# Performance work log

Measured on AMD Instinct MI355X. Metric: run time of the kernel, lower is better.

The kernel has to match this reference:

```python
import jax, jax.numpy as jnp
import numpy as np
from jax import lax


def run_gru(seq, w_ih, w_hh, b_ih, b_hh):
    """PyTorch-convention GRU. seq: (T, N, E) -> outputs (T, N, H), h0 = 0."""
    H = w_hh.shape[1]
    gx = jnp.einsum('tne,ge->tng', seq, w_ih) + b_ih  # (T, N, 3H), precomputed input gates

    def step(h, gx_t):
        gh = h @ w_hh.T + b_hh
        xr, xz, xn = jnp.split(gx_t, 3, axis=-1)
        hr, hz, hn = jnp.split(gh, 3, axis=-1)
        r = jax.nn.sigmoid(xr + hr)
        z = jax.nn.sigmoid(xz + hz)
        n = jnp.tanh(xn + r * hn)
        h_new = (1.0 - z) * n + z * h
        return h_new, h_new

    h0 = jnp.zeros((seq.shape[1], H), dtype=seq.dtype)
    _, hs = lax.scan(step, h0, gx)
    return hs


def setup_inputs() -> dict:
    key = jax.random.key(0)
    ks = jax.random.split(key, 20)
    B, T, I, E, Ha, Hb, O = 32, 64, 256, 256, 256, 256, 1
    s = 0.05
    return {
        'x': jax.random.normal(ks[0], (B, T, I), dtype=jnp.float32),
        'emb_w': jax.random.normal(ks[1], (E, I), dtype=jnp.float32) * s,
        'emb_b': jax.random.normal(ks[2], (E,), dtype=jnp.float32) * s,
        'a_wih': jax.random.normal(ks[3], (3 * Ha, E), dtype=jnp.float32) * s,
        'a_whh': jax.random.normal(ks[4], (3 * Ha, Ha), dtype=jnp.float32) * s,
        'a_bih': jax.random.normal(ks[5], (3 * Ha,), dtype=jnp.float32) * s,
        'a_bhh': jax.random.normal(ks[6], (3 * Ha,), dtype=jnp.float32) * s,
        'b_wih': jax.random.normal(ks[7], (3 * Hb, E), dtype=jnp.float32) * s,
        'b_whh': jax.random.normal(ks[8], (3 * Hb, Hb), dtype=jnp.float32) * s,
        'b_bih': jax.random.normal(ks[9], (3 * Hb,), dtype=jnp.float32) * s,
        'b_bhh': jax.random.normal(ks[10], (3 * Hb,), dtype=jnp.float32) * s,
        'alpha_w': jax.random.normal(ks[11], (1, Ha), dtype=jnp.float32) * s,
        'alpha_b': jax.random.normal(ks[12], (1,), dtype=jnp.float32) * s,
        'beta_w': jax.random.normal(ks[13], (E, Hb), dtype=jnp.float32) * s,
        'beta_b': jax.random.normal(ks[14], (E,), dtype=jnp.float32) * s,
        'out_w': jax.random.normal(ks[15], (O, E), dtype=jnp.float32) * s,
        'out_b': jax.random.normal(ks[16], (O,), dtype=jnp.float32) * s,
    }


def reference(x, emb_w, emb_b, a_wih, a_whh, a_bih, a_bhh,
              b_wih, b_whh, b_bih, b_bhh, alpha_w, alpha_b,
              beta_w, beta_b, out_w, out_b):
    B, T, I = x.shape
    P = T - 1  # prefix lengths 1..T-1
    xt = jnp.transpose(x, (1, 0, 2))               # (T, B, I) time-major
    emb = jnp.einsum('tbi,ei->tbe', xt, emb_w) + emb_b  # (T, B, E)
    E = emb.shape[-1]

    # Reversed prefix p (length t=p+1): rev[p, k] = emb[p - k] for k < t, else 0.
    idx = jnp.arange(P)[:, None] - jnp.arange(T)[None, :]   # (P, T)
    valid = idx >= 0
    idxc = jnp.clip(idx, 0)
    rev = jnp.where(valid[:, :, None, None], emb[idxc], 0.0)  # (P, T, B, E)

    seq = jnp.transpose(rev, (1, 0, 2, 3)).reshape(T, P * B, E)  # (T, P*B, E)
    ha = run_gru(seq, a_wih, a_whh, a_bih, a_bhh)  # (T, P*B, Ha)
    hb = run_gru(seq, b_wih, b_whh, b_bih, b_bhh)  # (T, P*B, Hb)
    ha = jnp.transpose(ha.reshape(T, P, B, -1), (1, 0, 2, 3))  # (P, T, B, Ha)
    hb = jnp.transpose(hb.reshape(T, P, B, -1), (1, 0, 2, 3))

    # flip back within each prefix (same index map), then * 0.5 as in the source
    rows = jnp.arange(P)[:, None]
    fa = ha[rows, idxc] * 0.5   # (P, T, B, Ha); positions >= t are junk, masked below
    fb = hb[rows, idxc] * 0.5

    pre = jnp.einsum('ptbh,h->ptb', fa, alpha_w[0]) + alpha_b[0]
    logits = jnp.where(valid[:, :, None], pre, -jnp.inf)
    alpha = jax.nn.softmax(logits, axis=1)                       # softmax over time per prefix
    beta = jnp.tanh(jnp.einsum('ptbh,eh->ptbe', fb, beta_w) + beta_b)  # (P, T, B, E)

    # context: c_t = sum_j alpha * beta * emb[:t]  (alpha is 0 outside prefix)
    c = jnp.einsum('ptb,ptbe,tbe->pbe', alpha, beta, emb)        # (P, B, E)
    pred = (c @ out_w.T + out_b)                                  # (P, B, 1)
    pred = jnp.transpose(pred, (1, 0, 2))                         # (B, P, 1)

    # contribution weights; w_emb / w_out enter via .data in torch (no grad)
    w_emb = lax.stop_gradient(emb_w)
    w_out0 = lax.stop_gradient(out_w)[0]
    e = jnp.einsum('ptbe,e,ei->ptbi', beta, w_out0, w_emb)        # (P, T, B, I)
    denom = jnp.arange(1, P + 1, dtype=x.dtype)[:, None, None]    # mean over t visits
    g = jnp.einsum('ptb,ptbi,tbi->pbi', alpha, e, xt) / denom     # (P, B, I)
    weight = jnp.transpose(g, (1, 0, 2))                          # (B, P, I)
    return pred, weight
```

## Files before the change

### kernel.cpp

```cpp
#include <hip/hip_runtime.h>
#include <math.h>

#define B_   32
#define T_   64
#define P_   63
#define E_   256

typedef _Float16 half8 __attribute__((ext_vector_type(8)));
typedef _Float16 half4 __attribute__((ext_vector_type(4)));
typedef float    f32x4 __attribute__((ext_vector_type(4)));

__device__ __forceinline__ float sigmoidf_(float x) { return 1.0f / (1.0f + __expf(-x)); }
__device__ __forceinline__ float tanhfast_(float x) { float e = __expf(2.0f*x); return 1.0f - 2.0f/(e + 1.0f); }

__device__ __forceinline__ void barrier_lds_() {
    asm volatile("" ::: "memory");
    asm volatile("s_waitcnt lgkmcnt(0)" ::: "memory");
    __builtin_amdgcn_s_barrier();
    asm volatile("" ::: "memory");
}

__global__ __launch_bounds__(64) void k_prep(
    const float* __restrict__ awhh, const float* __restrict__ bwhh,
    const float* __restrict__ awih, const float* __restrict__ bwih,
    const float* __restrict__ beta_w, const float* __restrict__ emb_w, const float* __restrict__ out_w,
    _Float16* __restrict__ wfa, _Float16* __restrict__ wfb,
    _Float16* __restrict__ wifa, _Float16* __restrict__ wifb,
    _Float16* __restrict__ bwf, _Float16* __restrict__ mf)
{
    int bid = blockIdx.x, l = threadIdx.x;
    if (bid < 1664) {
        const float* W; _Float16* dst; float scale = 1.0f; int r;
        if (bid < 384)       { W = awhh;   dst = wfa;  r = bid; }
        else if (bid < 768)  { W = bwhh;   dst = wfb;  r = bid - 384; }
        else if (bid < 1152) { W = awih;   dst = wifa; r = bid - 768; }
        else if (bid < 1536) { W = bwih;   dst = wifb; r = bid - 1152; }
        else                 { W = beta_w; dst = bwf;  r = bid - 1536; scale = 0.5f; }
        int ot = r >> 3, kc = r & 7;
        int orow = ot * 16 + (l & 15);
        int c0   = kc * 32 + (l >> 4) * 8;
        half8 v;
        #pragma unroll
        for (int j = 0; j < 8; ++j) v[j] = (_Float16)(scale * W[(size_t)orow * 256 + c0 + j]);
        *reinterpret_cast<half8*>(&dst[((size_t)r * 64 + l) * 8]) = v;
    } else {
        int r = bid - 1664;
        int ot = r >> 3, kc = r & 7;
        int i  = ot * 16 + (l & 15);
        int e0 = kc * 32 + (l >> 4) * 8;
        half8 v;
        #pragma unroll
        for (int j = 0; j < 8; ++j) v[j] = (_Float16)(out_w[e0 + j] * emb_w[(size_t)(e0 + j) * 256 + i]);
        *reinterpret_cast<half8*>(&mf[((size_t)r * 64 + l) * 8]) = v;
    }
}

__global__ __launch_bounds__(256) void k_emb(const float* __restrict__ x,
                                             const float* __restrict__ emb_w,
                                             const float* __restrict__ emb_b,
                                             const float* __restrict__ out_w,
                                             _Float16* __restrict__ embh,
                                             _Float16* __restrict__ ewh,
                                             _Float16* __restrict__ xh) {
    int r0 = blockIdx.x * 8;
    int tid = threadIdx.x;
    __shared__ float xs[8][E_];
    for (int rr = 0; rr < 8; ++rr) {
        int row = r0 + rr, t = row >> 5, b = row & 31;
        float xv = x[((size_t)b * T_ + t) * E_ + tid];
        xs[rr][tid] = xv;
        xh[((size_t)b * T_ + t) * E_ + tid] = (_Float16)xv;
    }
    __syncthreads();
    float acc[8];
    #pragma unroll
    for (int rr = 0; rr < 8; ++rr) acc[rr] = 0.f;
    const float* wr = emb_w + (size_t)tid * E_;
    for (int c = 0; c < 256; c += 4) {
        float4 wv = *reinterpret_cast<const float4*>(wr + c);
        #pragma unroll
        for (int rr = 0; rr < 8; ++rr) {
            float4 ev = *reinterpret_cast<const float4*>(&xs[rr][c]);
            acc[rr] += wv.x * ev.x + wv.y * ev.y + wv.z * ev.z + wv.w * ev.w;
        }
    }
    float eb = emb_b[tid], ow = out_w[tid];
    #pragma unroll
    for (int rr = 0; rr < 8; ++rr) {
        float v = acc[rr] + eb;
        embh[(size_t)(r0 + rr) * E_ + tid] = (_Float16)v;
        ewh[(size_t)(r0 + rr) * E_ + tid]  = (_Float16)(v * ow);
    }
}

__global__ __launch_bounds__(512, 2) void k_gates2(
    const _Float16* __restrict__ embh,
    const _Float16* __restrict__ wifa, const _Float16* __restrict__ wifb,
    const float* __restrict__ abih, const float* __restrict__ abhh,
    const float* __restrict__ bbih, const float* __restrict__ bbhh,
    _Float16* __restrict__ gpa, _Float16* __restrict__ gpb)
{
    __shared__ _Float16 esw[32 * E_];
    int bid = blockIdx.x;
    int g = bid >> 6, t = bid & 63;
    const _Float16* wif = g ? wifb : wifa;
    const float* bih = g ? bbih : abih;
    const float* bhh = g ? bbhh : abhh;
    _Float16* gp = g ? gpb : gpa;
    int tid = threadIdx.x, w = tid >> 6, l = tid & 63, lg = l >> 4, lr = l & 15;

    #pragma unroll
    for (int q = 0; q < 2; ++q) {
        int idx = q * 512 + tid;
        int b = idx >> 5, e0 = (idx & 31) * 8;
        half8 v = *reinterpret_cast<const half8*>(&embh[((size_t)t * 32 + b) * E_ + e0]);
        *reinterpret_cast<half8*>(&esw[b * E_ + (e0 ^ ((b & 7) << 3))]) = v;
    }
    half8 aw[3][2][8];
    #pragma unroll
    for (int g3 = 0; g3 < 3; ++g3)
        #pragma unroll
        for (int i = 0; i < 2; ++i)
            #pragma unroll
            for (int kc = 0; kc < 8; ++kc)
                aw[g3][i][kc] = *reinterpret_cast<const half8*>(
                    &wif[(((size_t)(g3 * 16 + 2 * w + i) * 8 + kc) * 64 + l) * 8]);
    f32x4 acc[3][2][2];
    #pragma unroll
    for (int g3 = 0; g3 < 3; ++g3)
        #pragma unroll
        for (int i = 0; i < 2; ++i)
            #pragma unroll
            for (int rt = 0; rt < 2; ++rt)
                #pragma unroll
                for (int j = 0; j < 4; ++j) {
                    int d = g3 * 256 + 32 * w + 16 * i + lg * 4 + j;
                    acc[g3][i][rt][j] = bih[d] + ((g3 < 2) ? bhh[d] : 0.f);
                }
    __syncthreads();
    #pragma unroll
    for (int kc = 0; kc < 8; ++kc) {
        half8 eb[2];
        #pragma unroll
        for (int rt = 0; rt < 2; ++rt)
            eb[rt] = *reinterpret_cast<const half8*>(
                &esw[(rt * 16 + lr) * E_ + ((kc * 32 + lg * 8) ^ ((lr & 7) << 3))]);
        #pragma unroll
        for (int g3 = 0; g3 < 3; ++g3)
            #pragma unroll
            for (int i = 0; i < 2; ++i)
                #pragma unroll
                for (int rt = 0; rt < 2; ++rt)
                    acc[g3][i][rt] = __builtin_amdgcn_mfma_f32_16x16x32_f16(
                        aw[g3][i][kc], eb[rt], acc[g3][i][rt], 0, 0, 0);
    }
    #pragma unroll
    for (int g3 = 0; g3 < 3; ++g3)
        #pragma unroll
        for (int rt = 0; rt < 2; ++rt) {
            half8 v;
            #pragma unroll
            for (int i = 0; i < 2; ++i)
                #pragma unroll
                for (int j = 0; j < 4; ++j) v[i * 4 + j] = (_Float16)acc[g3][i][rt][j];
            *reinterpret_cast<half8*>(
                &gp[((((size_t)t * 2 + rt) * 8 + w) * 3 + g3) * 512 + l * 8]) = v;
        }
}

__global__ __launch_bounds__(512, 2) void k_gru_f(
    const _Float16* __restrict__ gpa, const _Float16* __restrict__ gpb,
    const _Float16* __restrict__ wfa, const _Float16* __restrict__ wfb,
    const float* __restrict__ abhh, const float* __restrict__ bbhh,
    const float* __restrict__ alpha_w, const float* __restrict__ alpha_b,
    float* __restrict__ pre, _Float16* __restrict__ hstore)
{
    extern __shared__ char smem[];
    half8*    wlds = reinterpret_cast<half8*>(smem);
    _Float16* hsp  = reinterpret_cast<_Float16*>(smem + 98304);
    float*    red  = reinterpret_cast<float*>(smem + 98304 + 16384);

    int bid = blockIdx.x;
    int p   = 62 - (bid >> 2);
    int g   = (bid >> 1) & 1;
    int bh  = bid & 1;
    int tid = threadIdx.x;
    int w = tid >> 6, l = tid & 63, lg = l >> 4, lr = l & 15;
    const _Float16* gp  = g ? gpb : gpa;
    const _Float16* wf  = g ? wfb : wfa;
    const float*    bhh = g ? bbhh : abhh;

    half8 wreg[3][2][6];
    #pragma unroll
    for (int g3 = 0; g3 < 3; ++g3)
        #pragma unroll
        for (int i = 0; i < 2; ++i) {
            int ot = g3 * 16 + 2 * w + i;
            #pragma unroll
            for (int kc = 0; kc < 6; ++kc)
                wreg[g3][i][kc] = *reinterpret_cast<const half8*>(&wf[((size_t)(ot * 8 + kc) * 64 + l) * 8]);
        }
    #pragma unroll
    for (int q = 0; q < 12; ++q) {
        int idx = q * 512 + tid;
        int ot = idx >> 7, kcs = (idx >> 6) & 1, l2 = idx & 63;
        wlds[idx] = *reinterpret_cast<const half8*>(&wf[((size_t)(ot * 8 + 6 + kcs) * 64 + l2) * 8]);
    }
    float bhn[2][4], awv[2][4];
    #pragma unroll
    for (int i = 0; i < 2; ++i)
        #pragma unroll
        for (int j = 0; j < 4; ++j) {
            int d = 32 * w + 16 * i + lg * 4 + j;
            bhn[i][j] = bhh[512 + d];
            awv[i][j] = alpha_w[d];
        }
    float ab = alpha_b[0];
    float hreg[2][4];
    #pragma unroll
    for (int i = 0; i < 2; ++i)
        #pragma unroll
        for (int j = 0; j < 4; ++j) hreg[i][j] = 0.f;
    __syncthreads();

    size_t tri = (size_t)p * (p + 1) / 2;

    for (int k = 0; k <= p; ++k) {
        int t_in = p - k;
        int wr = k & 1, rb = wr ^ 1;
        if (k > 0 && g == 0 && tid < 16) {
            float s = 0.f;
            #pragma unroll
            for (int q = 0; q < 8; ++q) s += red[(rb * 16 + tid) * 8 + q];
            pre[((size_t)p * T_ + (t_in + 1)) * B_ + bh * 16 + tid] = 0.5f * s + ab;
        }
        half8 gch[3];
        {
            const _Float16* gq = gp + (((size_t)(t_in * 2 + bh) * 8 + w) * 3) * 512 + l * 8;
            #pragma unroll
            for (int c = 0; c < 3; ++c)
                gch[c] = *reinterpret_cast<const half8*>(gq + (size_t)c * 512);
        }
        f32x4 acc[3][2];
        #pragma unroll
        for (int g3 = 0; g3 < 3; ++g3)
            #pragma unroll
            for (int i = 0; i < 2; ++i)
                #pragma unroll
                for (int j = 0; j < 4; ++j) acc[g3][i][j] = 0.f;
        if (k > 0) {
            half8 bhv[2];
            {
                int cb = (lg * 8) ^ ((lr & 7) << 3);
                bhv[0] = *reinterpret_cast<const half8*>(&hsp[(rb * 16 + lr) * 256 + cb]);
            }
            #pragma unroll
            for (int kc = 0; kc < 8; ++kc) {
                if (kc < 7) {
                    int cb = ((kc + 1) * 32 + lg * 8) ^ ((lr & 7) << 3);
                    bhv[(kc + 1) & 1] = *reinterpret_cast<const half8*>(&hsp[(rb * 16 + lr) * 256 + cb]);
                }
                if (kc < 6) {
                    #pragma unroll
                    for (int g3 = 0; g3 < 3; ++g3)
                        #pragma unroll
                        for (int i = 0; i < 2; ++i)
                            acc[g3][i] = __builtin_amdgcn_mfma_f32_16x16x32_f16(
                                wreg[g3][i][kc], bhv[kc & 1], acc[g3][i], 0, 0, 0);
                } else {
                    #pragma unroll
                    for (int g3 = 0; g3 < 3; ++g3)
                        #pragma unroll
                        for (int i = 0; i < 2; ++i) {
                            half8 wlv = wlds[((g3 * 16 + 2 * w + i) * 2 + (kc - 6)) * 64 + l];
                            acc[g3][i] = __builtin_amdgcn_mfma_f32_16x16x32_f16(
                                wlv, bhv[kc & 1], acc[g3][i], 0, 0, 0);
                        }
                }
            }
        }
        _Float16* hdst = hstore + ((tri + (size_t)k) * B_ + bh * 16 + lr) * (size_t)E_ + 32 * w + lg * 4;
        #pragma unroll
        for (int i = 0; i < 2; ++i) {
            half4 hh;
            #pragma unroll
            for (int j = 0; j < 4; ++j) {
                int e = i * 4 + j;
                float rg = sigmoidf_(acc[0][i][j] + (float)gch[0][e]);
                float zg = sigmoidf_(acc[1][i][j] + (float)gch[1][e]);
                float ng = tanhfast_((float)gch[2][e] + rg * (acc[2][i][j] + bhn[i][j]));
                float h  = (1.f - zg) * ng + zg * hreg[i][j];
                hreg[i][j] = h;
                hh[j] = (_Float16)h;
            }
            int ce = (32 * w + 16 * i + lg * 4) ^ ((lr & 7) << 3);
            *reinterpret_cast<half4*>(&hsp[(wr * 16 + lr) * 256 + ce]) = hh;
            if (g) *reinterpret_cast<half4*>(hdst + 16 * i) = hh;
        }
        if (!g) {
            float pa = 0.f;
            #pragma unroll
            for (int i = 0; i < 2; ++i)
                #pragma unroll
                for (int j = 0; j < 4; ++j) pa += hreg[i][j] * awv[i][j];
            pa += __shfl_xor(pa, 16, 64);
            pa += __shfl_xor(pa, 32, 64);
            if (l < 16) red[(wr * 16 + l) * 8 + w] = pa;
        }
        barrier_lds_();
    }
    if (g == 0 && tid < 16) {
        int wl = p & 1;
        float s = 0.f;
        #pragma unroll
        for (int q = 0; q < 8; ++q) s += red[(wl * 16 + tid) * 8 + q];
        pre[((size_t)p * T_ + 0) * B_ + bh * 16 + tid] = 0.5f * s + ab;
    }
}

__global__ __launch_bounds__(512, 2) void k_att3(
    const _Float16* __restrict__ hH,
    const _Float16* __restrict__ bwf, const _Float16* __restrict__ mf,
    const float* __restrict__ beta_b,
    const float* __restrict__ pre,
    const _Float16* __restrict__ ewh, const _Float16* __restrict__ xh,
    const float* __restrict__ out_b,
    float* __restrict__ out)
{
    extern __shared__ char smem[];
    _Float16* hs   = reinterpret_cast<_Float16*>(smem);
    _Float16* es2  = reinterpret_cast<_Float16*>(smem + 32768);
    _Float16* xs2  = reinterpret_cast<_Float16*>(smem + 65536);
    float*    alds = reinterpret_cast<float*>(smem + 98304);
    float*    red2 = reinterpret_cast<float*>(smem + 98304 + 256);
    int tid = threadIdx.x, w = tid >> 6, l = tid & 63, lg = l >> 4, lr = l & 15;

    half8 aw2[2][8], am2[2][8];
    #pragma unroll
    for (int i = 0; i < 2; ++i)
        #pragma unroll
        for (int kc = 0; kc < 8; ++kc) {
            size_t fo = (((size_t)(2 * w + i) * 8 + kc) * 64 + l) * 8;
            aw2[i][kc] = *reinterpret_cast<const half8*>(&bwf[fo]);
            am2[i][kc] = *reinterpret_cast<const half8*>(&mf[fo]);
        }
    float bb2[2][4];
    #pragma unroll
    for (int i = 0; i < 2; ++i)
        #pragma unroll
        for (int j = 0; j < 4; ++j)
            bb2[i][j] = beta_b[(2 * w + i) * 16 + lg * 4 + j];
    float ob = out_b[0];

    for (int it = 0; it < 8; ++it) {
        int pair = blockIdx.x * 8 + it;
        int p = pair >> 5, b = pair & 31;
        size_t tri = (size_t)p * (p + 1) / 2;
        #pragma unroll
        for (int q = 0; q < 4; ++q) {
            int idx = q * 512 + tid;
            int k = idx >> 5, e0 = (idx & 31) * 8;
            int sw = e0 ^ ((k & 7) << 3);
            half8 hv, ev;
            if (k <= p) {
                hv = *reinterpret_cast<const half8*>(&hH[((tri + (size_t)(p - k)) * B_ + b) * 256 + e0]);
                ev = *reinterpret_cast<const half8*>(&ewh[((size_t)k * B_ + b) * 256 + e0]);
            } else {
                #pragma unroll
                for (int j = 0; j < 8; ++j) { hv[j] = (_Float16)0.f; ev[j] = (_Float16)0.f; }
            }
            *reinterpret_cast<half8*>(&hs[k * 256 + sw])  = hv;
            *reinterpret_cast<half8*>(&es2[k * 256 + sw]) = ev;
            *reinterpret_cast<half8*>(&xs2[k * 256 + sw]) =
                *reinterpret_cast<const half8*>(&xh[((size_t)b * T_ + k) * 256 + e0]);
        }
        if (tid < 64) {
            float v = (tid <= p) ? pre[((size_t)p * T_ + tid) * B_ + b] : -3.4e38f;
            float m = v;
            #pragma unroll
            for (int off = 32; off > 0; off >>= 1) m = fmaxf(m, __shfl_xor(m, off, 64));
            float e = (tid <= p) ? __expf(v - m) : 0.f;
            float s = e;
            #pragma unroll
            for (int off = 32; off > 0; off >>= 1) s += __shfl_xor(s, off, 64);
            alds[tid] = e / s;
        }
        __syncthreads();
        f32x4 acc2[2][4];
        #pragma unroll
        for (int i = 0; i < 2; ++i)
            #pragma unroll
            for (int rt = 0; rt < 4; ++rt)
                #pragma unroll
                for (int j = 0; j < 4; ++j) acc2[i][rt][j] = bb2[i][j];
        #pragma unroll
        for (int kc = 0; kc < 8; ++kc) {
            half8 hb[4];
            #pragma unroll
            for (int rt = 0; rt < 4; ++rt)
                hb[rt] = *reinterpret_cast<const half8*>(&hs[(rt * 16 + lr) * 256 + ((kc * 32 + lg * 8) ^ ((lr & 7) << 3))]);
            #pragma unroll
            for (int i = 0; i < 2; ++i)
                #pragma unroll
                for (int rt = 0; rt < 4; ++rt)
                    acc2[i][rt] = __builtin_amdgcn_mfma_f32_16x16x32_f16(aw2[i][kc], hb[rt], acc2[i][rt], 0, 0, 0);
        }
        float pv = 0.f;
        half4 ureg[2][4];
        #pragma unroll
        for (int i = 0; i < 2; ++i)
            #pragma unroll
            for (int rt = 0; rt < 4; ++rt) {
                int k = rt * 16 + lr;
                float al = alds[k];
                int d0 = (2 * w + i) * 16 + lg * 4;
                half4 ev4 = *reinterpret_cast<const half4*>(&es2[k * 256 + (d0 ^ ((lr & 7) << 3))]);
                #pragma unroll
                for (int j = 0; j < 4; ++j) {
                    float u = al * tanhfast_(acc2[i][rt][j]);
                    ureg[i][rt][j] = (_Float16)u;
                    pv += u * (float)ev4[j];
                }
            }
        __syncthreads();
        #pragma unroll
        for (int i = 0; i < 2; ++i)
            #pragma unroll
            for (int rt = 0; rt < 4; ++rt) {
                int k = rt * 16 + lr;
                int d0 = (2 * w + i) * 16 + lg * 4;
                *reinterpret_cast<half4*>(&hs[k * 256 + (d0 ^ ((lr & 7) << 3))]) = ureg[i][rt];
            }
        #pragma unroll
        for (int off = 1; off < 64; off <<= 1) pv += __shfl_xor(pv, off, 64);
        if (l == 0) red2[w] = pv;
        __syncthreads();
        if (tid == 0) {
            float s = 0.f;
            #pragma unroll
            for (int q = 0; q < 8; ++q) s += red2[q];
            out[(size_t)b * P_ + p] = s + ob;
        }
        f32x4 a2[2][4];
        #pragma unroll
        for (int i = 0; i < 2; ++i)
            #pragma unroll
            for (int rt = 0; rt < 4; ++rt)
                #pragma unroll
                for (int j = 0; j < 4; ++j) a2[i][rt][j] = 0.f;
        #pragma unroll
        for (int kc = 0; kc < 8; ++kc) {
            half8 ub[4];
            #pragma unroll
            for (int rt = 0; rt < 4; ++rt)
                ub[rt] = *reinterpret_cast<const half8*>(&hs[(rt * 16 + lr) * 256 + ((kc * 32 + lg * 8) ^ ((lr & 7) << 3))]);
            #pragma unroll
            for (int i = 0; i < 2; ++i)
                #pragma unroll
                for (int rt = 0; rt < 4; ++rt)
                    a2[i][rt] = __builtin_amdgcn_mfma_f32_16x16x32_f16(am2[i][kc], ub[rt], a2[i][rt], 0, 0, 0);
        }
        float r4[2][4];
        #pragma unroll
        for (int i = 0; i < 2; ++i)
            #pragma unroll
            for (int j = 0; j < 4; ++j) r4[i][j] = 0.f;
        #pragma unroll
        for (int i = 0; i < 2; ++i)
            #pragma unroll
            for (int rt = 0; rt < 4; ++rt) {
                int k = rt * 16 + lr;
                int i0 = (2 * w + i) * 16 + lg * 4;
                half4 xv4 = *reinterpret_cast<const half4*>(&xs2[k * 256 + (i0 ^ ((lr & 7) << 3))]);
                #pragma unroll
                for (int j = 0; j < 4; ++j) r4[i][j] += a2[i][rt][j] * (float)xv4[j];
            }
        #pragma unroll
        for (int off = 1; off < 16; off <<= 1)
            #pragma unroll
            for (int i = 0; i < 2; ++i)
                #pragma unroll
                for (int j = 0; j < 4; ++j) r4[i][j] += __shfl_xor(r4[i][j], off, 64);
        if (lr == 0) {
            float inv = 1.f / (float)(p + 1);
            #pragma unroll
            for (int i = 0; i < 2; ++i) {
                f32x4 v;
                #pragma unroll
                for (int j = 0; j < 4; ++j) v[j] = r4[i][j] * inv;
                *reinterpret_cast<f32x4*>(&out[2016 + ((size_t)b * P_ + p) * 256 + (2 * w + i) * 16 + lg * 4]) = v;
            }
        }
        __syncthreads();
    }
}

extern "C" void kernel_launch(void* const* d_in, const int* in_sizes, int n_in,
                              void* d_out, int out_size, void* d_ws, size_t ws_size,
                              hipStream_t stream) {
    const float* x       = (const float*)d_in[0];
    const float* emb_w   = (const float*)d_in[1];
    const float* emb_b   = (const float*)d_in[2];
    const float* a_wih   = (const float*)d_in[3];
    const float* a_whh   = (const float*)d_in[4];
    const float* a_bih   = (const float*)d_in[5];
    const float* a_bhh   = (const float*)d_in[6];
    const float* b_wih   = (const float*)d_in[7];
    const float* b_whh   = (const float*)d_in[8];
    const float* b_bih   = (const float*)d_in[9];
    const float* b_bhh   = (const float*)d_in[10];
    const float* alpha_w = (const float*)d_in[11];
    const float* alpha_b = (const float*)d_in[12];
    const float* beta_w  = (const float*)d_in[13];
    const float* beta_b  = (const float*)d_in[14];
    const float* out_w   = (const float*)d_in[15];
    const float* out_b   = (const float*)d_in[16];
    float* out = (float*)d_out;

    float* ws = (float*)d_ws;
    _Float16* embh = (_Float16*)ws;
    _Float16* ewh  = embh + 524288;
    _Float16* xh   = ewh  + 524288;
    _Float16* gpa  = xh   + 524288;
    _Float16* gpb  = gpa  + 1572864;
    float* pre     = (float*)(gpb + 1572864);
    _Float16* wfa  = (_Float16*)(pre + 129024);
    _Float16* wfb  = wfa + 196608;
    _Float16* wifa = wfb + 196608;
    _Float16* wifb = wifa + 196608;
    _Float16* bwf  = wifb + 196608;
    _Float16* mf   = bwf + 65536;
    _Float16* hH   = mf  + 65536;

    const int GRU_LDS = 98304 + 16384 + 1024;
    (void)hipFuncSetAttribute((const void*)k_gru_f,
                              hipFuncAttributeMaxDynamicSharedMemorySize, GRU_LDS);
    const int ATT_LDS = 98304 + 256 + 32;
    (void)hipFuncSetAttribute((const void*)k_att3,
                              hipFuncAttributeMaxDynamicSharedMemorySize, ATT_LDS);

    k_prep<<<1792, 64, 0, stream>>>(a_whh, b_whh, a_wih, b_wih, beta_w, emb_w, out_w,
                                    wfa, wfb, wifa, wifb, bwf, mf);
    k_emb<<<256, 256, 0, stream>>>(x, emb_w, emb_b, out_w, embh, ewh, xh);
    k_gates2<<<128, 512, 0, stream>>>(embh, wifa, wifb, a_bih, a_bhh, b_bih, b_bhh, gpa, gpb);
    k_gru_f<<<252, 512, GRU_LDS, stream>>>(gpa, gpb, wfa, wfb, a_bhh, b_bhh,
                                           alpha_w, alpha_b, pre, hH);
    k_att3<<<252, 512, ATT_LDS, stream>>>(hH, bwf, mf, beta_b, pre, ewh, xh, out_b, out);
}
```

Baseline: 287.0 us.

## Prefetch next pair's global tiles into registers during attention compute

Inside the attention kernel, the global loads of hidden states, ewh, x and pre-logits for the next (prefix, batch) pair are issued into registers right after the first barrier. They then overlap with the current pair's MFMA and reduction work. The __syncthreads calls are replaced with a custom barrier that waits only on LDS counters, so in-flight global loads are not drained at each barrier. This adds about 12 half8 registers per thread, which may pressure occupancy under the 512x2 launch bound.

Result: slower. 333.5 us (+16.2%).

```diff
diff --git a/kernel.cpp b/kernel.cpp
--- a/kernel.cpp
+++ b/kernel.cpp
@@ -318,7 +318,7 @@
     }
 }
 
-__global__ __launch_bounds__(512, 2) void k_att3(
+__global__ __launch_bounds__(512, 2) void k_att4(
     const _Float16* __restrict__ hH,
     const _Float16* __restrict__ bwf, const _Float16* __restrict__ mf,
     const float* __restrict__ beta_b,
@@ -352,30 +352,48 @@
             bb2[i][j] = beta_b[(2 * w + i) * 16 + lg * 4 + j];
     float ob = out_b[0];
 
+    half8 sh[4], se[4], sx[4];
+    float spre;
+
+#define ISSUE(PAIR) do {                                                              \
+    int p_ = (PAIR) >> 5, b_ = (PAIR) & 31;                                           \
+    size_t tri_ = (size_t)p_ * (p_ + 1) / 2;                                          \
+    _Pragma("unroll")                                                                 \
+    for (int q_ = 0; q_ < 4; ++q_) {                                                  \
+        int idx_ = q_ * 512 + tid;                                                    \
+        int k_ = idx_ >> 5, e0_ = (idx_ & 31) * 8;                                    \
+        if (k_ <= p_) {                                                               \
+            sh[q_] = *reinterpret_cast<const half8*>(                                 \
+                &hH[((tri_ + (size_t)(p_ - k_)) * B_ + b_) * 256 + e0_]);             \
+            se[q_] = *reinterpret_cast<const half8*>(                                 \
+                &ewh[((size_t)k_ * B_ + b_) * 256 + e0_]);                            \
+        } else {                                                                      \
+            _Pragma("unroll")                                                         \
+            for (int j_ = 0; j_ < 8; ++j_) { sh[q_][j_] = (_Float16)0.f;              \
+                                             se[q_][j_] = (_Float16)0.f; }            \
+        }                                                                             \
+        sx[q_] = *reinterpret_cast<const half8*>(                                     \
+            &xh[((size_t)b_ * T_ + k_) * 256 + e0_]);                                 \
+    }                                                                                 \
+    spre = (tid < 64 && tid <= p_) ? pre[((size_t)p_ * T_ + tid) * B_ + b_] : -3.4e38f; \
+} while (0)
+
+    ISSUE(blockIdx.x * 8);
+
     for (int it = 0; it < 8; ++it) {
         int pair = blockIdx.x * 8 + it;
         int p = pair >> 5, b = pair & 31;
-        size_t tri = (size_t)p * (p + 1) / 2;
         #pragma unroll
         for (int q = 0; q < 4; ++q) {
             int idx = q * 512 + tid;
             int k = idx >> 5, e0 = (idx & 31) * 8;
             int sw = e0 ^ ((k & 7) << 3);
-            half8 hv, ev;
-            if (k <= p) {
-                hv = *reinterpret_cast<const half8*>(&hH[((tri + (size_t)(p - k)) * B_ + b) * 256 + e0]);
-                ev = *reinterpret_cast<const half8*>(&ewh[((size_t)k * B_ + b) * 256 + e0]);
-            } else {
-                #pragma unroll
-                for (int j = 0; j < 8; ++j) { hv[j] = (_Float16)0.f; ev[j] = (_Float16)0.f; }
-            }
-            *reinterpret_cast<half8*>(&hs[k * 256 + sw])  = hv;
-            *reinterpret_cast<half8*>(&es2[k * 256 + sw]) = ev;
-            *reinterpret_cast<half8*>(&xs2[k * 256 + sw]) =
-                *reinterpret_cast<const half8*>(&xh[((size_t)b * T_ + k) * 256 + e0]);
+            *reinterpret_cast<half8*>(&hs[k * 256 + sw])  = sh[q];
+            *reinterpret_cast<half8*>(&es2[k * 256 + sw]) = se[q];
+            *reinterpret_cast<half8*>(&xs2[k * 256 + sw]) = sx[q];
         }
         if (tid < 64) {
-            float v = (tid <= p) ? pre[((size_t)p * T_ + tid) * B_ + b] : -3.4e38f;
+            float v = spre;
             float m = v;
             #pragma unroll
             for (int off = 32; off > 0; off >>= 1) m = fmaxf(m, __shfl_xor(m, off, 64));
@@ -385,7 +403,8 @@
             for (int off = 32; off > 0; off >>= 1) s += __shfl_xor(s, off, 64);
             alds[tid] = e / s;
         }
-        __syncthreads();
+        barrier_lds_();
+        if (it < 7) ISSUE(pair + 1);
         f32x4 acc2[2][4];
         #pragma unroll
         for (int i = 0; i < 2; ++i)
@@ -422,7 +441,7 @@
                     pv += u * (float)ev4[j];
                 }
             }
-        __syncthreads();
+        barrier_lds_();
         #pragma unroll
         for (int i = 0; i < 2; ++i)
             #pragma unroll
@@ -434,7 +453,7 @@
         #pragma unroll
         for (int off = 1; off < 64; off <<= 1) pv += __shfl_xor(pv, off, 64);
         if (l == 0) red2[w] = pv;
-        __syncthreads();
+        barrier_lds_();
         if (tid == 0) {
             float s = 0.f;
             #pragma unroll
@@ -491,8 +510,9 @@
                 *reinterpret_cast<f32x4*>(&out[2016 + ((size_t)b * P_ + p) * 256 + (2 * w + i) * 16 + lg * 4]) = v;
             }
         }
-        __syncthreads();
-    }
+        barrier_lds_();
+    }
+#undef ISSUE
 }
 
 extern "C" void kernel_launch(void* const* d_in, const int* in_sizes, int n_in,
@@ -536,7 +556,7 @@
     (void)hipFuncSetAttribute((const void*)k_gru_f,
                               hipFuncAttributeMaxDynamicSharedMemorySize, GRU_LDS);
     const int ATT_LDS = 98304 + 256 + 32;
-    (void)hipFuncSetAttribute((const void*)k_att3,
+    (void)hipFuncSetAttribute((const void*)k_att4,
                               hipFuncAttributeMaxDynamicSharedMemorySize, ATT_LDS);
 
     k_prep<<<1792, 64, 0, stream>>>(a_whh, b_whh, a_wih, b_wih, beta_w, emb_w, out_w,
@@ -545,5 +565,5 @@
     k_gates2<<<128, 512, 0, stream>>>(embh, wifa, wifb, a_bih, a_bhh, b_bih, b_bhh, gpa, gpb);
     k_gru_f<<<252, 512, GRU_LDS, stream>>>(gpa, gpb, wfa, wfb, a_bhh, b_bhh,
                                            alpha_w, alpha_b, pre, hH);
-    k_att3<<<252, 512, ATT_LDS, stream>>>(hH, bwf, mf, beta_b, pre, ewh, xh, out_b, out);
-}
+    k_att4<<<252, 512, ATT_LDS, stream>>>(hH, bwf, mf, beta_b, pre, ewh, xh, out_b, out);
+}
```

## Process full batch per GRU block instead of splitting batch halves

Applied to the files above, without the earlier changes.

Each k_gru_f block now handles all 32 batch rows (two 16-row tiles) rather than one half, halving the grid from 252 to 126 blocks. The recurrent weights held in registers and LDS are reused across both row tiles, which doubles MFMA work per weight load and halves redundant weight staging. The gate-precompute layout in k_gates2 is permuted so that both row tiles sit next to each other, and LDS for hidden state and the reduction buffer is doubled. The trade-off is fewer blocks to fill the CUs and a longer serial time per block, plus higher register pressure from the doubled accumulators.

Result: slower. 582.5 us (+102.9%).

```diff
diff --git a/kernel.cpp b/kernel.cpp
--- a/kernel.cpp
+++ b/kernel.cpp
@@ -164,7 +164,7 @@
                 #pragma unroll
                 for (int j = 0; j < 4; ++j) v[i * 4 + j] = (_Float16)acc[g3][i][rt][j];
             *reinterpret_cast<half8*>(
-                &gp[((((size_t)t * 2 + rt) * 8 + w) * 3 + g3) * 512 + l * 8]) = v;
+                &gp[((((size_t)t * 8 + w) * 3 + g3) * 2 + rt) * 512 + l * 8]) = v;
         }
 }
 
@@ -178,12 +178,11 @@
     extern __shared__ char smem[];
     half8*    wlds = reinterpret_cast<half8*>(smem);
     _Float16* hsp  = reinterpret_cast<_Float16*>(smem + 98304);
-    float*    red  = reinterpret_cast<float*>(smem + 98304 + 16384);
+    float*    red  = reinterpret_cast<float*>(smem + 98304 + 32768);
 
     int bid = blockIdx.x;
-    int p   = 62 - (bid >> 2);
-    int g   = (bid >> 1) & 1;
-    int bh  = bid & 1;
+    int g   = bid / 63;
+    int p   = 62 - (bid % 63);
     int tid = threadIdx.x;
     int w = tid >> 6, l = tid & 63, lg = l >> 4, lr = l & 15;
     const _Float16* gp  = g ? gpb : gpa;
@@ -216,11 +215,13 @@
             awv[i][j] = alpha_w[d];
         }
     float ab = alpha_b[0];
-    float hreg[2][4];
+    float hreg[2][2][4];
     #pragma unroll
     for (int i = 0; i < 2; ++i)
         #pragma unroll
-        for (int j = 0; j < 4; ++j) hreg[i][j] = 0.f;
+        for (int rt = 0; rt < 2; ++rt)
+            #pragma unroll
+            for (int j = 0; j < 4; ++j) hreg[i][rt][j] = 0.f;
     __syncthreads();
 
     size_t tri = (size_t)p * (p + 1) / 2;
@@ -228,93 +229,111 @@
     for (int k = 0; k <= p; ++k) {
         int t_in = p - k;
         int wr = k & 1, rb = wr ^ 1;
-        if (k > 0 && g == 0 && tid < 16) {
+        if (k > 0 && g == 0 && tid < 32) {
             float s = 0.f;
             #pragma unroll
-            for (int q = 0; q < 8; ++q) s += red[(rb * 16 + tid) * 8 + q];
-            pre[((size_t)p * T_ + (t_in + 1)) * B_ + bh * 16 + tid] = 0.5f * s + ab;
-        }
-        half8 gch[3];
+            for (int q = 0; q < 8; ++q) s += red[(rb * 32 + tid) * 8 + q];
+            pre[((size_t)p * T_ + (t_in + 1)) * B_ + tid] = 0.5f * s + ab;
+        }
+        half8 gch[3][2];
         {
-            const _Float16* gq = gp + (((size_t)(t_in * 2 + bh) * 8 + w) * 3) * 512 + l * 8;
+            const _Float16* gq = gp + (((size_t)(t_in * 8 + w) * 3) * 2) * 512 + l * 8;
             #pragma unroll
             for (int c = 0; c < 3; ++c)
-                gch[c] = *reinterpret_cast<const half8*>(gq + (size_t)c * 512);
-        }
-        f32x4 acc[3][2];
+                #pragma unroll
+                for (int rt = 0; rt < 2; ++rt)
+                    gch[c][rt] = *reinterpret_cast<const half8*>(gq + (size_t)(c * 2 + rt) * 512);
+        }
+        f32x4 acc[3][2][2];
         #pragma unroll
         for (int g3 = 0; g3 < 3; ++g3)
             #pragma unroll
             for (int i = 0; i < 2; ++i)
                 #pragma unroll
-                for (int j = 0; j < 4; ++j) acc[g3][i][j] = 0.f;
+                for (int rt = 0; rt < 2; ++rt)
+                    #pragma unroll
+                    for (int j = 0; j < 4; ++j) acc[g3][i][rt][j] = 0.f;
         if (k > 0) {
-            half8 bhv[2];
-            {
+            half8 bhv[2][2];
+            #pragma unroll
+            for (int rt = 0; rt < 2; ++rt) {
                 int cb = (lg * 8) ^ ((lr & 7) << 3);
-                bhv[0] = *reinterpret_cast<const half8*>(&hsp[(rb * 16 + lr) * 256 + cb]);
+                bhv[0][rt] = *reinterpret_cast<const half8*>(&hsp[(rb * 32 + rt * 16 + lr) * 256 + cb]);
             }
             #pragma unroll
             for (int kc = 0; kc < 8; ++kc) {
                 if (kc < 7) {
-                    int cb = ((kc + 1) * 32 + lg * 8) ^ ((lr & 7) << 3);
-                    bhv[(kc + 1) & 1] = *reinterpret_cast<const half8*>(&hsp[(rb * 16 + lr) * 256 + cb]);
+                    #pragma unroll
+                    for (int rt = 0; rt < 2; ++rt) {
+                        int cb = ((kc + 1) * 32 + lg * 8) ^ ((lr & 7) << 3);
+                        bhv[(kc + 1) & 1][rt] = *reinterpret_cast<const half8*>(&hsp[(rb * 32 + rt * 16 + lr) * 256 + cb]);
+                    }
                 }
                 if (kc < 6) {
                     #pragma unroll
                     for (int g3 = 0; g3 < 3; ++g3)
                         #pragma unroll
                         for (int i = 0; i < 2; ++i)
-                            acc[g3][i] = __builtin_amdgcn_mfma_f32_16x16x32_f16(
-                                wreg[g3][i][kc], bhv[kc & 1], acc[g3][i], 0, 0, 0);
+                            #pragma unroll
+                            for (int rt = 0; rt < 2; ++rt)
+                                acc[g3][i][rt] = __builtin_amdgcn_mfma_f32_16x16x32_f16(
+                                    wreg[g3][i][kc], bhv[kc & 1][rt], acc[g3][i][rt], 0, 0, 0);
                 } else {
                     #pragma unroll
                     for (int g3 = 0; g3 < 3; ++g3)
                         #pragma unroll
                         for (int i = 0; i < 2; ++i) {
                             half8 wlv = wlds[((g3 * 16 + 2 * w + i) * 2 + (kc - 6)) * 64 + l];
-                            acc[g3][i] = __builtin_amdgcn_mfma_f32_16x16x32_f16(
-                                wlv, bhv[kc & 1], acc[g3][i], 0, 0, 0);
+                            #pragma unroll
+                            for (int rt = 0; rt < 2; ++rt)
+                                acc[g3][i][rt] = __builtin_amdgcn_mfma_f32_16x16x32_f16(
+                                    wlv, bhv[kc & 1][rt], acc[g3][i][rt], 0, 0, 0);
                         }
                 }
             }
         }
-        _Float16* hdst = hstore + ((tri + (size_t)k) * B_ + bh * 16 + lr) * (size_t)E_ + 32 * w + lg * 4;
-        #pragma unroll
-        for (int i = 0; i < 2; ++i) {
-            half4 hh;
-            #pragma unroll
-            for (int j = 0; j < 4; ++j) {
-                int e = i * 4 + j;
-                float rg = sigmoidf_(acc[0][i][j] + (float)gch[0][e]);
-                float zg = sigmoidf_(acc[1][i][j] + (float)gch[1][e]);
-                float ng = tanhfast_((float)gch[2][e] + rg * (acc[2][i][j] + bhn[i][j]));
-                float h  = (1.f - zg) * ng + zg * hreg[i][j];
-                hreg[i][j] = h;
-                hh[j] = (_Float16)h;
-            }
-            int ce = (32 * w + 16 * i + lg * 4) ^ ((lr & 7) << 3);
-            *reinterpret_cast<half4*>(&hsp[(wr * 16 + lr) * 256 + ce]) = hh;
-            if (g) *reinterpret_cast<half4*>(hdst + 16 * i) = hh;
+        #pragma unroll
+        for (int rt = 0; rt < 2; ++rt) {
+            _Float16* hdst = hstore + ((tri + (size_t)k) * B_ + rt * 16 + lr) * (size_t)E_ + 32 * w + lg * 4;
+            #pragma unroll
+            for (int i = 0; i < 2; ++i) {
+                half4 hh;
+                #pragma unroll
+                for (int j = 0; j < 4; ++j) {
+                    int e = i * 4 + j;
+                    float rg = sigmoidf_(acc[0][i][rt][j] + (float)gch[0][rt][e]);
+                    float zg = sigmoidf_(acc[1][i][rt][j] + (float)gch[1][rt][e]);
+                    float ng = tanhfast_((float)gch[2][rt][e] + rg * (acc[2][i][rt][j] + bhn[i][j]));
+                    float h  = (1.f - zg) * ng + zg * hreg[i][rt][j];
+                    hreg[i][rt][j] = h;
+                    hh[j] = (_Float16)h;
+                }
+                int ce = (32 * w + 16 * i + lg * 4) ^ ((lr & 7) << 3);
+                *reinterpret_cast<half4*>(&hsp[(wr * 32 + rt * 16 + lr) * 256 + ce]) = hh;
+                if (g) *reinterpret_cast<half4*>(hdst + 16 * i) = hh;
+            }
         }
         if (!g) {
-            float pa = 0.f;
-            #pragma unroll
-            for (int i = 0; i < 2; ++i)
-                #pragma unroll
-                for (int j = 0; j < 4; ++j) pa += hreg[i][j] * awv[i][j];
-            pa += __shfl_xor(pa, 16, 64);
-            pa += __shfl_xor(pa, 32, 64);
-            if (l < 16) red[(wr * 16 + l) * 8 + w] = pa;
+            #pragma unroll
+            for (int rt = 0; rt < 2; ++rt) {
+                float pa = 0.f;
+                #pragma unroll
+                for (int i = 0; i < 2; ++i)
+                    #pragma unroll
+                    for (int j = 0; j < 4; ++j) pa += hreg[i][rt][j] * awv[i][j];
+                pa += __shfl_xor(pa, 16, 64);
+                pa += __shfl_xor(pa, 32, 64);
+                if (l < 16) red[(wr * 32 + rt * 16 + l) * 8 + w] = pa;
+            }
         }
         barrier_lds_();
     }
-    if (g == 0 && tid < 16) {
+    if (g == 0 && tid < 32) {
         int wl = p & 1;
         float s = 0.f;
         #pragma unroll
-        for (int q = 0; q < 8; ++q) s += red[(wl * 16 + tid) * 8 + q];
-        pre[((size_t)p * T_ + 0) * B_ + bh * 16 + tid] = 0.5f * s + ab;
+        for (int q = 0; q < 8; ++q) s += red[(wl * 32 + tid) * 8 + q];
+        pre[((size_t)p * T_ + 0) * B_ + tid] = 0.5f * s + ab;
     }
 }
 
@@ -532,7 +551,7 @@
     _Float16* mf   = bwf + 65536;
     _Float16* hH   = mf  + 65536;
 
-    const int GRU_LDS = 98304 + 16384 + 1024;
+    const int GRU_LDS = 98304 + 32768 + 2048;
     (void)hipFuncSetAttribute((const void*)k_gru_f,
                               hipFuncAttributeMaxDynamicSharedMemorySize, GRU_LDS);
     const int ATT_LDS = 98304 + 256 + 32;
@@ -543,7 +562,7 @@
                                     wfa, wfb, wifa, wifb, bwf, mf);
     k_emb<<<256, 256, 0, stream>>>(x, emb_w, emb_b, out_w, embh, ewh, xh);
     k_gates2<<<128, 512, 0, stream>>>(embh, wifa, wifb, a_bih, a_bhh, b_bih, b_bhh, gpa, gpb);
-    k_gru_f<<<252, 512, GRU_LDS, stream>>>(gpa, gpb, wfa, wfb, a_bhh, b_bhh,
+    k_gru_f<<<126, 512, GRU_LDS, stream>>>(gpa, gpb, wfa, wfb, a_bhh, b_bhh,
                                            alpha_w, alpha_b, pre, hH);
     k_att3<<<252, 512, ATT_LDS, stream>>>(hH, bwf, mf, beta_b, pre, ewh, xh, out_b, out);
 }
```
